# Kernel optimization log

Measured on AMD Instinct MI355X. Metric: run time of the kernel, lower is better.

The kernel has to match this reference:

```python
import jax, jax.numpy as jnp
import numpy as np
from jax import lax

C_RED = 32
IN_CH = 256
BN_EPS = 1e-5
NORM_EPS = 1e-6


def setup_inputs() -> dict:
    key = jax.random.key(0)
    ks = jax.random.split(key, 5)
    B, H, W = 16, 64, 64
    x = jax.random.normal(ks[0], (B, IN_CH, H, W), dtype=jnp.float32)
    w_reduce = jax.random.normal(ks[1], (C_RED, IN_CH), dtype=jnp.float32) * 0.05
    bn_gamma = jnp.ones((C_RED,), dtype=jnp.float32)
    bn_beta = jnp.zeros((C_RED,), dtype=jnp.float32)
    bn_mean = jax.random.normal(ks[2], (C_RED,), dtype=jnp.float32) * 0.1
    bn_var = jax.random.uniform(ks[3], (C_RED,), dtype=jnp.float32, minval=0.5, maxval=1.5)
    # depthwise 3x3 kernel, OIHW with I=1 (groups == channels)
    dw_weight = jax.random.normal(ks[4], (C_RED, 1, 3, 3), dtype=jnp.float32) * 0.1
    scale = jnp.ones((C_RED,), dtype=jnp.float32)
    return {"x": x, "w_reduce": w_reduce, "bn_gamma": bn_gamma, "bn_beta": bn_beta,
            "bn_mean": bn_mean, "bn_var": bn_var, "dw_weight": dw_weight, "scale": scale}


def _l2_normalize(t):
    # F.normalize(p=2, dim=1, eps=1e-6): divide by max(||t||_2, eps) along channel dim
    n = jnp.sqrt(jnp.sum(t * t, axis=1, keepdims=True))
    return t / jnp.maximum(n, NORM_EPS)


def reference(x, w_reduce, bn_gamma, bn_beta, bn_mean, bn_var, dw_weight, scale):
    # 1x1 reduce conv (no bias)
    z = jnp.einsum('bihw,oi->bohw', x, w_reduce)
    # BatchNorm2d (inference: running stats)
    inv = bn_gamma / jnp.sqrt(bn_var + BN_EPS)
    z = z * inv[None, :, None, None] + (bn_beta - bn_mean * inv)[None, :, None, None]
    z = jax.nn.relu(z)
    # SpiralTwist: depthwise 3x3 conv (SAME) then per-channel scale
    z_tw = lax.conv_general_dilated(
        z, dw_weight, window_strides=(1, 1), padding='SAME',
        feature_group_count=C_RED,
        dimension_numbers=('NCHW', 'OIHW', 'NCHW'))
    z_tw = z_tw * scale[None, :, None, None]
    z_norm = _l2_normalize(z)
    z_tw_norm = _l2_normalize(z_tw)
    # upper-triangular channel pairs (i <= j)
    idx_i, idx_j = np.triu_indices(C_RED, k=0)
    pair = z_norm[:, idx_i] * z_tw_norm[:, idx_j]  # [B, C*(C+1)/2, H, W]
    return jnp.concatenate([z_norm, pair], axis=1)
```

## Files before the change

### kernel.cpp

```cpp
#include <hip/hip_runtime.h>
#include <stdint.h>

#define CIN  256
#define CR   32
#define COUT 560

__global__ __launch_bounds__(512) void k_conv1x1(
    const float* __restrict__ x,
    const float* __restrict__ wr,
    const float* __restrict__ gamma,
    const float* __restrict__ beta,
    const float* __restrict__ mean,
    const float* __restrict__ var,
    float* __restrict__ z)
{
    const int tid = threadIdx.x;
    const int og  = __builtin_amdgcn_readfirstlane(tid >> 6);
    const int q   = tid & 63;
    const int blk = blockIdx.x;
    const int b   = blk >> 4;
    const int p0  = (blk & 15) << 8;

    const float* xb = x + ((((size_t)b) * CIN) << 12) + p0 + (q << 2);
    const float* wp = wr + og * 4 * CIN;

    float4 a0 = {0.f,0.f,0.f,0.f};
    float4 a1 = {0.f,0.f,0.f,0.f};
    float4 a2 = {0.f,0.f,0.f,0.f};
    float4 a3 = {0.f,0.f,0.f,0.f};

    #pragma unroll 2
    for (int cc = 0; cc < 16; ++cc) {
        float4 xv[16];
        #pragma unroll
        for (int k = 0; k < 16; ++k)
            xv[k] = *(const float4*)(xb + ((size_t)(cc * 16 + k) << 12));
        #pragma unroll
        for (int k = 0; k < 16; ++k) {
            const int ic = cc * 16 + k;
            const float w0 = wp[           ic];
            const float w1 = wp[    CIN  + ic];
            const float w2 = wp[2 * CIN  + ic];
            const float w3 = wp[3 * CIN  + ic];
            a0.x = fmaf(xv[k].x, w0, a0.x);
            a0.y = fmaf(xv[k].y, w0, a0.y);
            a0.z = fmaf(xv[k].z, w0, a0.z);
            a0.w = fmaf(xv[k].w, w0, a0.w);
            a1.x = fmaf(xv[k].x, w1, a1.x);
            a1.y = fmaf(xv[k].y, w1, a1.y);
            a1.z = fmaf(xv[k].z, w1, a1.z);
            a1.w = fmaf(xv[k].w, w1, a1.w);
            a2.x = fmaf(xv[k].x, w2, a2.x);
            a2.y = fmaf(xv[k].y, w2, a2.y);
            a2.z = fmaf(xv[k].z, w2, a2.z);
            a2.w = fmaf(xv[k].w, w2, a2.w);
            a3.x = fmaf(xv[k].x, w3, a3.x);
            a3.y = fmaf(xv[k].y, w3, a3.y);
            a3.z = fmaf(xv[k].z, w3, a3.z);
            a3.w = fmaf(xv[k].w, w3, a3.w);
        }
    }

    float4* zq = (float4*)(z + (((size_t)b * CR) << 12) + p0 + (q << 2));
    #pragma unroll
    for (int o = 0; o < 4; ++o) {
        const int oc = og * 4 + o;
        const float inv = gamma[oc] / sqrtf(var[oc] + 1e-5f);
        const float bia = beta[oc] - mean[oc] * inv;
        const float4 a = (o == 0) ? a0 : (o == 1) ? a1 : (o == 2) ? a2 : a3;
        float4 r;
        r.x = fmaxf(fmaf(a.x, inv, bia), 0.f);
        r.y = fmaxf(fmaf(a.y, inv, bia), 0.f);
        r.z = fmaxf(fmaf(a.z, inv, bia), 0.f);
        r.w = fmaxf(fmaf(a.w, inv, bia), 0.f);
        zq[(size_t)oc << 10] = r;
    }
}

__global__ __launch_bounds__(256) void k_twist(
    const float* __restrict__ z,
    const float* __restrict__ dww,
    const float* __restrict__ scl,
    float* __restrict__ out)
{
    __shared__ float4 znl4[CR][64];
    __shared__ float4 ps1[4][64];
    __shared__ float4 ps2[4][64];

    const int tid  = threadIdx.x;
    const int cg   = __builtin_amdgcn_readfirstlane(tid >> 6);
    const int lane = tid & 63;
    const int r    = lane >> 4;
    const int cq   = lane & 15;
    const int blk  = blockIdx.x;
    const int b    = blk >> 4;
    const int h0   = (blk & 15) << 2;
    const int hh   = h0 + r;

    const float* zb = z + (((size_t)b * CR) << 12);

    float4 zc[8], tw[8];
    float4 s1 = {0.f,0.f,0.f,0.f};
    float4 s2 = {0.f,0.f,0.f,0.f};

    #pragma unroll
    for (int k = 0; k < 8; ++k) {
        const int c = cg + 4 * k;
        const float* zp = zb + ((size_t)c << 12);
        float4 acc = {0.f,0.f,0.f,0.f};
        float4 ctr = {0.f,0.f,0.f,0.f};
        #pragma unroll
        for (int dy = 0; dy < 3; ++dy) {
            const int hy = hh + dy - 1;
            const bool rok = ((unsigned)hy) < 64u;
            const float* zr = zp + (hy << 6);
            float4 M  = {0.f,0.f,0.f,0.f};
            float4 L4 = {0.f,0.f,0.f,0.f};
            float4 R4 = {0.f,0.f,0.f,0.f};
            if (rok) {
                M = *(const float4*)(zr + (cq << 2));
                if (cq > 0)  L4 = *(const float4*)(zr + (cq << 2) - 4);
                if (cq < 15) R4 = *(const float4*)(zr + (cq << 2) + 4);
            }
            const float w0 = dww[c * 9 + dy * 3 + 0];
            const float w1 = dww[c * 9 + dy * 3 + 1];
            const float w2 = dww[c * 9 + dy * 3 + 2];
            acc.x = fmaf(w0, L4.w, fmaf(w1, M.x, fmaf(w2, M.y, acc.x)));
            acc.y = fmaf(w0, M.x,  fmaf(w1, M.y, fmaf(w2, M.z, acc.y)));
            acc.z = fmaf(w0, M.y,  fmaf(w1, M.z, fmaf(w2, M.w, acc.z)));
            acc.w = fmaf(w0, M.z,  fmaf(w1, M.w, fmaf(w2, R4.x, acc.w)));
            if (dy == 1) ctr = M;
        }
        const float s = scl[c];
        float4 t;
        t.x = acc.x * s;  t.y = acc.y * s;  t.z = acc.z * s;  t.w = acc.w * s;
        zc[k] = ctr;  tw[k] = t;
        s1.x = fmaf(ctr.x, ctr.x, s1.x);  s1.y = fmaf(ctr.y, ctr.y, s1.y);
        s1.z = fmaf(ctr.z, ctr.z, s1.z);  s1.w = fmaf(ctr.w, ctr.w, s1.w);
        s2.x = fmaf(t.x, t.x, s2.x);      s2.y = fmaf(t.y, t.y, s2.y);
        s2.z = fmaf(t.z, t.z, s2.z);      s2.w = fmaf(t.w, t.w, s2.w);
    }

    ps1[cg][lane] = s1;
    ps2[cg][lane] = s2;
    __syncthreads();

    float4 t1, t2;
    {
        const float4 u0 = ps1[0][lane], u1 = ps1[1][lane],
                     u2 = ps1[2][lane], u3 = ps1[3][lane];
        t1.x = u0.x + u1.x + u2.x + u3.x;  t1.y = u0.y + u1.y + u2.y + u3.y;
        t1.z = u0.z + u1.z + u2.z + u3.z;  t1.w = u0.w + u1.w + u2.w + u3.w;
        const float4 v0 = ps2[0][lane], v1 = ps2[1][lane],
                     v2 = ps2[2][lane], v3 = ps2[3][lane];
        t2.x = v0.x + v1.x + v2.x + v3.x;  t2.y = v0.y + v1.y + v2.y + v3.y;
        t2.z = v0.z + v1.z + v2.z + v3.z;  t2.w = v0.w + v1.w + v2.w + v3.w;
    }
    float4 rn1, rn2;
    rn1.x = 1.0f / fmaxf(sqrtf(t1.x), 1e-6f);
    rn1.y = 1.0f / fmaxf(sqrtf(t1.y), 1e-6f);
    rn1.z = 1.0f / fmaxf(sqrtf(t1.z), 1e-6f);
    rn1.w = 1.0f / fmaxf(sqrtf(t1.w), 1e-6f);
    rn2.x = 1.0f / fmaxf(sqrtf(t2.x), 1e-6f);
    rn2.y = 1.0f / fmaxf(sqrtf(t2.y), 1e-6f);
    rn2.z = 1.0f / fmaxf(sqrtf(t2.z), 1e-6f);
    rn2.w = 1.0f / fmaxf(sqrtf(t2.w), 1e-6f);

    float4* outq = (float4*)(out + (((size_t)b * COUT) << 12) + (hh << 6)) + cq;

    #pragma unroll
    for (int k = 0; k < 8; ++k) {
        const int c = cg + 4 * k;
        float4 zn;
        zn.x = zc[k].x * rn1.x;  zn.y = zc[k].y * rn1.y;
        zn.z = zc[k].z * rn1.z;  zn.w = zc[k].w * rn1.w;
        outq[(size_t)c << 10] = zn;
        znl4[c][lane] = zn;
        tw[k].x *= rn2.x;  tw[k].y *= rn2.y;
        tw[k].z *= rn2.z;  tw[k].w *= rn2.w;
    }
    __syncthreads();

    #pragma unroll
    for (int k = 0; k < 8; ++k) {
        const int j = cg + 4 * k;
        const float4 t = tw[k];
        int P = 32 + j;
        for (int i = 0; i <= j; ++i) {
            const float4 zi = znl4[i][lane];
            float4 v;
            v.x = zi.x * t.x;  v.y = zi.y * t.y;
            v.z = zi.z * t.z;  v.w = zi.w * t.w;
            outq[(size_t)P << 10] = v;
            P += 31 - i;
        }
    }
}

extern "C" void kernel_launch(void* const* d_in, const int* in_sizes, int n_in,
                              void* d_out, int out_size, void* d_ws, size_t ws_size,
                              hipStream_t stream) {
    const float* x     = (const float*)d_in[0];
    const float* wr    = (const float*)d_in[1];
    const float* gamma = (const float*)d_in[2];
    const float* beta  = (const float*)d_in[3];
    const float* mean  = (const float*)d_in[4];
    const float* var   = (const float*)d_in[5];
    const float* dww   = (const float*)d_in[6];
    const float* scl   = (const float*)d_in[7];
    float* z   = (float*)d_ws;
    float* out = (float*)d_out;

    hipLaunchKernelGGL(k_conv1x1, dim3(256), dim3(512), 0, stream,
                       x, wr, gamma, beta, mean, var, z);
    hipLaunchKernelGGL(k_twist, dim3(256), dim3(256), 0, stream,
                       z, dww, scl, out);
}
```

Before: 225.1 us.

## Split twist pair writes across 4x more blocks and double-buffer conv loads

New measurement: 234.7 us. 1.04x slower.

```diff
diff --git a/kernel.cpp b/kernel.cpp
--- a/kernel.cpp
+++ b/kernel.cpp
@@ -29,37 +29,41 @@
     float4 a2 = {0.f,0.f,0.f,0.f};
     float4 a3 = {0.f,0.f,0.f,0.f};
 
-    #pragma unroll 2
-    for (int cc = 0; cc < 16; ++cc) {
-        float4 xv[16];
-        #pragma unroll
-        for (int k = 0; k < 16; ++k)
-            xv[k] = *(const float4*)(xb + ((size_t)(cc * 16 + k) << 12));
-        #pragma unroll
-        for (int k = 0; k < 16; ++k) {
-            const int ic = cc * 16 + k;
-            const float w0 = wp[           ic];
-            const float w1 = wp[    CIN  + ic];
-            const float w2 = wp[2 * CIN  + ic];
-            const float w3 = wp[3 * CIN  + ic];
-            a0.x = fmaf(xv[k].x, w0, a0.x);
-            a0.y = fmaf(xv[k].y, w0, a0.y);
-            a0.z = fmaf(xv[k].z, w0, a0.z);
-            a0.w = fmaf(xv[k].w, w0, a0.w);
-            a1.x = fmaf(xv[k].x, w1, a1.x);
-            a1.y = fmaf(xv[k].y, w1, a1.y);
-            a1.z = fmaf(xv[k].z, w1, a1.z);
-            a1.w = fmaf(xv[k].w, w1, a1.w);
-            a2.x = fmaf(xv[k].x, w2, a2.x);
-            a2.y = fmaf(xv[k].y, w2, a2.y);
-            a2.z = fmaf(xv[k].z, w2, a2.z);
-            a2.w = fmaf(xv[k].w, w2, a2.w);
-            a3.x = fmaf(xv[k].x, w3, a3.x);
-            a3.y = fmaf(xv[k].y, w3, a3.y);
-            a3.z = fmaf(xv[k].z, w3, a3.z);
-            a3.w = fmaf(xv[k].w, w3, a3.w);
-        }
-    }
+    float4 xv0[16], xv1[16];
+
+#define LOADCH(buf, cc)                                                      \
+    _Pragma("unroll")                                                        \
+    for (int k = 0; k < 16; ++k)                                             \
+        buf[k] = *(const float4*)(xb + ((size_t)((cc) * 16 + k) << 12));
+
+#define FMACH(buf, cc)                                                       \
+    _Pragma("unroll")                                                        \
+    for (int k = 0; k < 16; ++k) {                                           \
+        const int ic = (cc) * 16 + k;                                        \
+        const float w0 = wp[           ic];                                  \
+        const float w1 = wp[    CIN  + ic];                                  \
+        const float w2 = wp[2 * CIN  + ic];                                  \
+        const float w3 = wp[3 * CIN  + ic];                                  \
+        a0.x = fmaf(buf[k].x, w0, a0.x);  a0.y = fmaf(buf[k].y, w0, a0.y);   \
+        a0.z = fmaf(buf[k].z, w0, a0.z);  a0.w = fmaf(buf[k].w, w0, a0.w);   \
+        a1.x = fmaf(buf[k].x, w1, a1.x);  a1.y = fmaf(buf[k].y, w1, a1.y);   \
+        a1.z = fmaf(buf[k].z, w1, a1.z);  a1.w = fmaf(buf[k].w, w1, a1.w);   \
+        a2.x = fmaf(buf[k].x, w2, a2.x);  a2.y = fmaf(buf[k].y, w2, a2.y);   \
+        a2.z = fmaf(buf[k].z, w2, a2.z);  a2.w = fmaf(buf[k].w, w2, a2.w);   \
+        a3.x = fmaf(buf[k].x, w3, a3.x);  a3.y = fmaf(buf[k].y, w3, a3.y);   \
+        a3.z = fmaf(buf[k].z, w3, a3.z);  a3.w = fmaf(buf[k].w, w3, a3.w);   \
+    }
+
+    LOADCH(xv0, 0);
+    #pragma unroll 1
+    for (int cc = 0; cc < 16; cc += 2) {
+        LOADCH(xv1, cc + 1);
+        FMACH(xv0, cc);
+        if (cc + 2 < 16) { LOADCH(xv0, cc + 2); }
+        FMACH(xv1, cc + 1);
+    }
+#undef LOADCH
+#undef FMACH
 
     float4* zq = (float4*)(z + (((size_t)b * CR) << 12) + p0 + (q << 2));
     #pragma unroll
@@ -93,8 +97,10 @@
     const int r    = lane >> 4;
     const int cq   = lane & 15;
     const int blk  = blockIdx.x;
-    const int b    = blk >> 4;
-    const int h0   = (blk & 15) << 2;
+    const int qq   = blk & 3;
+    const int sl   = blk >> 2;
+    const int b    = sl >> 4;
+    const int h0   = (sl & 15) << 2;
     const int hh   = h0 + r;
 
     const float* zb = z + (((size_t)b * CR) << 12);
@@ -174,8 +180,8 @@
         float4 zn;
         zn.x = zc[k].x * rn1.x;  zn.y = zc[k].y * rn1.y;
         zn.z = zc[k].z * rn1.z;  zn.w = zc[k].w * rn1.w;
-        outq[(size_t)c << 10] = zn;
         znl4[c][lane] = zn;
+        if (qq == 0) outq[(size_t)c << 10] = zn;
         tw[k].x *= rn2.x;  tw[k].y *= rn2.y;
         tw[k].z *= rn2.z;  tw[k].w *= rn2.w;
     }
@@ -185,8 +191,10 @@
     for (int k = 0; k < 8; ++k) {
         const int j = cg + 4 * k;
         const float4 t = tw[k];
-        int P = 32 + j;
-        for (int i = 0; i <= j; ++i) {
+        const int i0 = (qq * (j + 1)) >> 2;
+        const int i1 = ((qq + 1) * (j + 1)) >> 2;
+        int P = 32 + j + 31 * i0 - ((i0 * (i0 - 1)) >> 1);
+        for (int i = i0; i < i1; ++i) {
             const float4 zi = znl4[i][lane];
             float4 v;
             v.x = zi.x * t.x;  v.y = zi.y * t.y;
@@ -213,6 +221,6 @@
 
     hipLaunchKernelGGL(k_conv1x1, dim3(256), dim3(512), 0, stream,
                        x, wr, gamma, beta, mean, var, z);
-    hipLaunchKernelGGL(k_twist, dim3(256), dim3(256), 0, stream,
+    hipLaunchKernelGGL(k_twist, dim3(1024), dim3(256), 0, stream,
                        z, dww, scl, out);
 }
```
